# Optimization experiments

Hardware: AMD Instinct MI355X
Metric: run time of the kernel (lower is better)

## Reference

```python
import jax, jax.numpy as jnp
import numpy as np

L_V, L_T, D, H, HID = 1024, 128, 4096, 8, 2048
N1 = L_V // 2      # tokens kept by selector module 1
N2 = N1 // 2       # tokens kept by selector module 2 (final selected)
N_REM = L_V - N2   # remaining tokens to merge


def setup_inputs() -> dict:
    key = jax.random.key(0)
    ks = jax.random.split(key, 8)
    s = 0.02
    return {
        "vision_feature": jax.random.normal(ks[0], (L_V, D), jnp.float32),
        "text_embed": jax.random.normal(ks[1], (L_T, D), jnp.float32),
        "attention_mask": jnp.ones((L_T,), jnp.int32),
        # stacked MHA params, order: [m1.global, m1.local, m2.global, m2.local]
        "attn_in_w": s * jax.random.normal(ks[2], (4, 3 * D, D), jnp.float32),
        "attn_in_b": jnp.zeros((4, 3 * D), jnp.float32),
        "attn_out_w": s * jax.random.normal(ks[3], (4, D, D), jnp.float32),
        "attn_out_b": jnp.zeros((4, D), jnp.float32),
        # stacked MLP params, order: [module1, module2]
        "mlp_w1": s * jax.random.normal(ks[4], (2, HID, D), jnp.float32),
        "mlp_b1": jnp.zeros((2, HID), jnp.float32),
        "mlp_w2": s * jax.random.normal(ks[5], (2, HID), jnp.float32),
        "mlp_b2": jnp.zeros((2,), jnp.float32),
    }


def _mha(xq, xkv, in_w, in_b, out_w, out_b):
    # torch nn.MultiheadAttention (unbatched, eval mode: no dropout)
    dh = D // H
    qw, kw, vw = jnp.split(in_w, 3, axis=0)
    qb, kb, vb = jnp.split(in_b, 3)
    q = (xq @ qw.T + qb).reshape(-1, H, dh)
    k = (xkv @ kw.T + kb).reshape(-1, H, dh)
    v = (xkv @ vw.T + vb).reshape(-1, H, dh)
    scores = jnp.einsum('qhd,khd->hqk', q, k) * (1.0 / np.sqrt(dh))
    attn = jax.nn.softmax(scores, axis=-1)
    o = jnp.einsum('hqk,khd->qhd', attn, v).reshape(-1, D)
    return o @ out_w.T + out_b


def _select(vf, te, pg, pl, w1, b1, w2, b2, n_keep):
    # TokenSelectionModule (deterministic top-k selection path, fixed shapes)
    comb = jnp.concatenate([vf, te], axis=0)
    g = _mha(vf, comb, *pg)
    l = _mha(vf, te, *pl) + vf
    x = jnp.stack([l, g], axis=1)                      # (L, 2, D): 0=local, 1=global
    h = jax.nn.relu(jnp.einsum('lcd,hd->lch', x, w1) + b1)
    logits = jnp.einsum('lch,h->lc', h, w2) + b2       # (L, 2)
    _, idx = jax.lax.top_k(logits[:, 1], n_keep)
    return vf[idx], idx


def _forward(vision_feature, text_embed, attn_in_w, attn_in_b, attn_out_w,
             attn_out_b, mlp_w1, mlp_b1, mlp_w2, mlp_b2):
    p = lambda i: (attn_in_w[i], attn_in_b[i], attn_out_w[i], attn_out_b[i])
    sv1, idx1 = _select(vision_feature, text_embed, p(0), p(1),
                        mlp_w1[0], mlp_b1[0], mlp_w2[0], mlp_b2[0], N1)
    sel, idx2 = _select(sv1, text_embed, p(2), p(3),
                        mlp_w1[1], mlp_b1[1], mlp_w2[1], mlp_b2[1], N2)
    sel_idx = idx1[idx2]

    # remaining = complement of selected indices (fixed size N_REM)
    sel_mask = jnp.zeros((L_V,), bool).at[sel_idx].set(True)
    rem_idx = jnp.nonzero(~sel_mask, size=N_REM)[0]
    rem = vision_feature[rem_idx]                      # (N_REM, D)

    # cosine similarity (torch eps=1e-8) + argmax matching
    nr = jnp.linalg.norm(rem, axis=-1)
    ns = jnp.linalg.norm(sel, axis=-1)
    sim = (rem @ sel.T) / jnp.maximum(nr[:, None] * ns[None, :], 1e-8)
    best = jnp.argmax(sim, axis=1)                     # (N_REM,) cluster ids

    # per-cluster gather+mean+normalize merge, vectorized as segment reduces
    cnt = jax.ops.segment_sum(jnp.ones((N_REM,), jnp.float32), best, num_segments=N2)
    sum_rem = jax.ops.segment_sum(rem, best, num_segments=N2)
    mean = (sel + sum_rem) / (cnt + 1.0)[:, None]
    seg_max = jax.ops.segment_max(nr, best, num_segments=N2)
    max_norm = jnp.maximum(ns, jnp.where(cnt > 0, seg_max, 0.0))
    mean_unit = mean / jnp.linalg.norm(mean, axis=-1, keepdims=True)
    updated = jnp.where((cnt > 0)[:, None], mean_unit * max_norm[:, None], sel)
    return updated  # top_k == 0 path: return merged selected features


def reference(vision_feature, text_embed, attention_mask, attn_in_w, attn_in_b,
              attn_out_w, attn_out_b, mlp_w1, mlp_b1, mlp_w2, mlp_b2):
    # attention_mask is accepted but unused, matching the torch forward
    return _forward(vision_feature, text_embed, attn_in_w, attn_in_b,
                    attn_out_w, attn_out_b, mlp_w1, mlp_b1, mlp_w2, mlp_b2)
```

## Files before the change

kernel.cpp:

```cpp
#include <hip/hip_runtime.h>
#include <hip/hip_bf16.h>
#include <math.h>
#include <stdint.h>

typedef __attribute__((ext_vector_type(4))) float f32x4;
typedef __attribute__((ext_vector_type(8))) short s16x8;
typedef __attribute__((ext_vector_type(4))) short s16x4;

struct sh2 { short hi, lo; };

__device__ __forceinline__ sh2 splitf(float x)
{
    __hip_bfloat16 h = __float2bfloat16(x);
    float hf = __bfloat162float(h);
    __hip_bfloat16 l = __float2bfloat16(x - hf);
    sh2 r;
    r.hi = __builtin_bit_cast(short, h);
    r.lo = __builtin_bit_cast(short, l);
    return r;
}

__device__ __forceinline__ void split8(const float4& a, const float4& b,
                                       s16x8& h, s16x8& l)
{
    sh2 p;
    p = splitf(a.x); h[0] = p.hi; l[0] = p.lo;
    p = splitf(a.y); h[1] = p.hi; l[1] = p.lo;
    p = splitf(a.z); h[2] = p.hi; l[2] = p.lo;
    p = splitf(a.w); h[3] = p.hi; l[3] = p.lo;
    p = splitf(b.x); h[4] = p.hi; l[4] = p.lo;
    p = splitf(b.y); h[5] = p.hi; l[5] = p.lo;
    p = splitf(b.z); h[6] = p.hi; l[6] = p.lo;
    p = splitf(b.w); h[7] = p.hi; l[7] = p.lo;
}

typedef const __attribute__((address_space(1))) void gvoid_t;
typedef __attribute__((address_space(3))) void lvoid_t;
__device__ __forceinline__ void gld_lds16(const void* g, void* l)
{
    __builtin_amdgcn_global_load_lds((gvoid_t*)(uintptr_t)g,
                                     (lvoid_t*)(uintptr_t)l, 16, 0, 0);
}

template<int BF, int EPI, bool RELU>
__global__ __launch_bounds__(256, 2) void mfma_gemm(
    const short* __restrict__ Ahi, const short* __restrict__ Alo, int lda, long sA,
    const float* __restrict__ Bf, const short* __restrict__ Bhi,
    const short* __restrict__ Blo, int ldb, long sB,
    float* __restrict__ Cf, short* __restrict__ Chi, short* __restrict__ Clo,
    short* __restrict__ Thi, short* __restrict__ Tlo, int ldc, int ldT, long sC,
    int K, int SK, float alpha, const float* __restrict__ bias, int mskip)
{
    __shared__ short SH[2][16384];
    const int zf = blockIdx.z;
    const int sk = (SK > 1) ? (zf % SK) : 0;
    const int bz = (SK > 1) ? (zf / SK) : zf;
    const int Kc = K / SK;
    const int kb = sk * Kc;
    Ahi += (long)bz * sA; Alo += (long)bz * sA;
    if (BF == 0) Bf += (long)bz * sB; else { Bhi += (long)bz * sB; Blo += (long)bz * sB; }
    const long cofs = (long)((SK > 1) ? zf : bz) * sC;

    const int GX = gridDim.x, GY = gridDim.y;
    const int nwg = GX * GY;
    const int bid = blockIdx.x + GX * blockIdx.y;
    const int q8 = nwg >> 3, r8 = nwg & 7;
    const int xcd = bid & 7, sl = bid >> 3;
    const int t = (xcd < r8) ? (xcd * (q8 + 1) + sl)
                             : (r8 * (q8 + 1) + (xcd - r8) * q8 + sl);
    const int m0 = (t % GY) * 128, n0 = (t / GY) * 128;

    if (EPI == 2 && n0 < 4096 && m0 >= mskip) return;

    const int tid = threadIdx.x;
    const int lane = tid & 63, wave = tid >> 6;
    const int wr = (wave >> 1) * 64, wc = (wave & 1) * 64;
    const int lrow = lane & 15, lk = lane >> 4;
    const int cswz8 = (lk ^ ((lrow >> 1) & 3)) << 3;

    const int rA0 = wave * 16 + (lane >> 2);
    const int rA1 = rA0 + 64;
    const int sc0 = ((lane & 3) ^ ((rA0 >> 1) & 3)) * 8;
    const int sc1 = ((lane & 3) ^ ((rA1 >> 1) & 3)) * 8;
    const long gA0 = (long)(m0 + rA0) * lda + sc0;
    const long gA1 = (long)(m0 + rA1) * lda + sc1;
    long gB0 = 0, gB1 = 0;
    if (BF == 1) {
        gB0 = (long)(n0 + rA0) * ldb + sc0;
        gB1 = (long)(n0 + rA1) * ldb + sc1;
    }
    const int lw0 = wave * 512, lw1 = wave * 512 + 2048;

    const int brow = tid & 127;
    const int bkc0 = (tid >> 7) * 8;
    const int bkc1 = bkc0 + 16;
    const int bw0 = brow * 32 + (((bkc0 >> 3) ^ ((brow >> 1) & 3)) << 3);
    const int bw1 = brow * 32 + (((bkc1 >> 3) ^ ((brow >> 1) & 3)) << 3);
    const float* bpr = (BF == 0) ? Bf + (long)(n0 + brow) * ldb : nullptr;

    f32x4 acc[4][4];
#pragma unroll
    for (int i = 0; i < 4; i++)
#pragma unroll
        for (int j = 0; j < 4; j++) acc[i][j] = (f32x4){0.f, 0.f, 0.f, 0.f};

    float4 rb0a, rb0b, rb1a, rb1b;

    {
        short* S = &SH[0][0];
        gld_lds16(Ahi + gA0 + kb, S + lw0);
        gld_lds16(Ahi + gA1 + kb, S + lw1);
        gld_lds16(Alo + gA0 + kb, S + 4096 + lw0);
        gld_lds16(Alo + gA1 + kb, S + 4096 + lw1);
        if constexpr (BF == 1) {
            gld_lds16(Bhi + gB0 + kb, S + 8192 + lw0);
            gld_lds16(Bhi + gB1 + kb, S + 8192 + lw1);
            gld_lds16(Blo + gB0 + kb, S + 12288 + lw0);
            gld_lds16(Blo + gB1 + kb, S + 12288 + lw1);
        } else {
            rb0a = *(const float4*)(bpr + kb + bkc0);
            rb0b = *(const float4*)(bpr + kb + bkc0 + 4);
            rb1a = *(const float4*)(bpr + kb + bkc1);
            rb1b = *(const float4*)(bpr + kb + bkc1 + 4);
            s16x8 h, l;
            split8(rb0a, rb0b, h, l);
            *(s16x8*)&S[8192 + bw0] = h;
            *(s16x8*)&S[12288 + bw0] = l;
            split8(rb1a, rb1b, h, l);
            *(s16x8*)&S[8192 + bw1] = h;
            *(s16x8*)&S[12288 + bw1] = l;
        }
    }
    __syncthreads();

    int cur = 0;
    const int kend = kb + Kc;
    for (int k0 = kb; k0 < kend; k0 += 32) {
        const int kn = k0 + 32;
        const bool nx = (kn < kend);
        short* SN = &SH[cur ^ 1][0];
        if (nx) {
            gld_lds16(Ahi + gA0 + kn, SN + lw0);
            gld_lds16(Ahi + gA1 + kn, SN + lw1);
            gld_lds16(Alo + gA0 + kn, SN + 4096 + lw0);
            gld_lds16(Alo + gA1 + kn, SN + 4096 + lw1);
            if constexpr (BF == 1) {
                gld_lds16(Bhi + gB0 + kn, SN + 8192 + lw0);
                gld_lds16(Bhi + gB1 + kn, SN + 8192 + lw1);
                gld_lds16(Blo + gB0 + kn, SN + 12288 + lw0);
                gld_lds16(Blo + gB1 + kn, SN + 12288 + lw1);
            } else {
                rb0a = *(const float4*)(bpr + kn + bkc0);
                rb0b = *(const float4*)(bpr + kn + bkc0 + 4);
                rb1a = *(const float4*)(bpr + kn + bkc1);
                rb1b = *(const float4*)(bpr + kn + bkc1 + 4);
            }
        }
        const short* S = &SH[cur][0];
        s16x8 ah[4], al[4], bh[4], bl[4];
#pragma unroll
        for (int m = 0; m < 4; m++) {
            const int idx = (wr + m * 16 + lrow) * 32 + cswz8;
            ah[m] = *(const s16x8*)&S[idx];
            al[m] = *(const s16x8*)&S[4096 + idx];
        }
#pragma unroll
        for (int n = 0; n < 4; n++) {
            const int idx = (wc + n * 16 + lrow) * 32 + cswz8;
            bh[n] = *(const s16x8*)&S[8192 + idx];
            bl[n] = *(const s16x8*)&S[12288 + idx];
        }
#pragma unroll
        for (int n = 0; n < 4; n++)
#pragma unroll
            for (int m = 0; m < 4; m++)
                acc[m][n] = __builtin_amdgcn_mfma_f32_16x16x32_bf16(ah[m], bh[n], acc[m][n], 0, 0, 0);
#pragma unroll
        for (int n = 0; n < 4; n++)
#pragma unroll
            for (int m = 0; m < 4; m++)
                acc[m][n] = __builtin_amdgcn_mfma_f32_16x16x32_bf16(ah[m], bl[n], acc[m][n], 0, 0, 0);
#pragma unroll
        for (int n = 0; n < 4; n++)
#pragma unroll
            for (int m = 0; m < 4; m++)
                acc[m][n] = __builtin_amdgcn_mfma_f32_16x16x32_bf16(al[m], bh[n], acc[m][n], 0, 0, 0);
        if (BF == 0 && nx) {
            s16x8 h, l;
            split8(rb0a, rb0b, h, l);
            *(s16x8*)&SN[8192 + bw0] = h;
            *(s16x8*)&SN[12288 + bw0] = l;
            split8(rb1a, rb1b, h, l);
            *(s16x8*)&SN[8192 + bw1] = h;
            *(s16x8*)&SN[12288 + bw1] = l;
        }
        __syncthreads();
        cur ^= 1;
    }
#pragma unroll
    for (int n = 0; n < 4; n++) {
        const int col = n0 + wc + n * 16 + lrow;
        const float bv = (SK == 1 && bias) ? bias[col] : 0.f;
#pragma unroll
        for (int m = 0; m < 4; m++) {
            const int row = m0 + wr + m * 16 + lk * 4;
            if (SK > 1) {
#pragma unroll
                for (int r = 0; r < 4; r++)
                    Cf[cofs + (long)(row + r) * ldc + col] = acc[m][n][r] * alpha;
            } else if constexpr (EPI == 0) {
#pragma unroll
                for (int r = 0; r < 4; r++) {
                    float v = acc[m][n][r] * alpha + bv;
                    if (RELU) v = fmaxf(v, 0.f);
                    Cf[cofs + (long)(row + r) * ldc + col] = v;
                }
            } else if constexpr (EPI == 1) {
#pragma unroll
                for (int r = 0; r < 4; r++) {
                    float v = acc[m][n][r] * alpha + bv;
                    sh2 p = splitf(v);
                    Chi[cofs + (long)(row + r) * ldc + col] = p.hi;
                    Clo[cofs + (long)(row + r) * ldc + col] = p.lo;
                }
            } else {
                if (n0 < 8192) {
#pragma unroll
                    for (int r = 0; r < 4; r++) {
                        float v = acc[m][n][r] + bv;
                        sh2 p = splitf(v);
                        Chi[(long)(row + r) * ldc + col] = p.hi;
                        Clo[(long)(row + r) * ldc + col] = p.lo;
                    }
                } else {
                    s16x4 h4, l4;
#pragma unroll
                    for (int r = 0; r < 4; r++) {
                        float v = acc[m][n][r] + bv;
                        sh2 p = splitf(v);
                        h4[r] = p.hi; l4[r] = p.lo;
                    }
                    const long tof = (long)(col - 8192) * ldT + row;
                    *(s16x4*)&Thi[tof] = h4;
                    *(s16x4*)&Tlo[tof] = l4;
                }
            }
        }
    }
}

__global__ __launch_bounds__(512, 2) void mfma_gemm256(
    const short* __restrict__ Ahi, const short* __restrict__ Alo, int lda,
    const float* __restrict__ Bf, int ldb,
    short* __restrict__ Chi, short* __restrict__ Clo,
    short* __restrict__ Thi, short* __restrict__ Tlo, int ldc, int ldT,
    int K, int Mreal, const float* __restrict__ bias, int mskip)
{
    __shared__ short SH[2][32768];

    const int GX = gridDim.x, GY = gridDim.y;
    const int nwg = GX * GY;
    const int bid = blockIdx.x + GX * blockIdx.y;
    const int q8 = nwg >> 3, r8 = nwg & 7;
    const int xcd = bid & 7, sl = bid >> 3;
    const int t = (xcd < r8) ? (xcd * (q8 + 1) + sl)
                             : (r8 * (q8 + 1) + (xcd - r8) * q8 + sl);
    const int m0 = (t % GY) * 256, n0 = (t / GY) * 256;

    if (n0 < 4096 && m0 >= mskip) return;

    const int tid = threadIdx.x;
    const int lane = tid & 63, wave = tid >> 6;
    const int wr = (wave >> 1) * 64, wc = (wave & 1) * 128;
    const int lrow = lane & 15, lk = lane >> 4;
    const int cswz8 = (lk ^ ((lrow >> 1) & 3)) << 3;

    const int rA0 = wave * 32 + (lane >> 2);
    const int rA1 = rA0 + 16;
    const int sc0 = ((lane & 3) ^ ((rA0 >> 1) & 3)) * 8;
    const int sc1 = ((lane & 3) ^ ((rA1 >> 1) & 3)) * 8;
    const long gA0 = (long)(m0 + rA0) * lda + sc0;
    const long gA1 = (long)(m0 + rA1) * lda + sc1;
    const int lw0 = wave * 1024, lw1 = wave * 1024 + 512;

    const int brow = tid & 255;
    const int bk = (tid >> 8) * 16;
    const int bw0 = brow * 32 + ((((bk >> 3) + 0) ^ ((brow >> 1) & 3)) << 3);
    const int bw1 = brow * 32 + ((((bk >> 3) + 1) ^ ((brow >> 1) & 3)) << 3);
    const float* bpr = Bf + (long)(n0 + brow) * ldb + bk;

    f32x4 acc[4][8];
#pragma unroll
    for (int i = 0; i < 4; i++)
#pragma unroll
        for (int j = 0; j < 8; j++) acc[i][j] = (f32x4){0.f, 0.f, 0.f, 0.f};

    float4 rb0, rb1, rb2, rb3;

    {
        short* S = &SH[0][0];
        gld_lds16(Ahi + gA0, S + lw0);
        gld_lds16(Ahi + gA1, S + lw1);
        gld_lds16(Alo + gA0, S + 8192 + lw0);
        gld_lds16(Alo + gA1, S + 8192 + lw1);
        rb0 = *(const float4*)(bpr + 0);
        rb1 = *(const float4*)(bpr + 4);
        rb2 = *(const float4*)(bpr + 8);
        rb3 = *(const float4*)(bpr + 12);
        s16x8 h, l;
        split8(rb0, rb1, h, l);
        *(s16x8*)&S[16384 + bw0] = h;
        *(s16x8*)&S[24576 + bw0] = l;
        split8(rb2, rb3, h, l);
        *(s16x8*)&S[16384 + bw1] = h;
        *(s16x8*)&S[24576 + bw1] = l;
    }
    __syncthreads();

    int cur = 0;
    for (int k0 = 0; k0 < K; k0 += 32) {
        const int kn = k0 + 32;
        const bool nx = (kn < K);
        short* SN = &SH[cur ^ 1][0];
        if (nx) {
            gld_lds16(Ahi + gA0 + kn, SN + lw0);
            gld_lds16(Ahi + gA1 + kn, SN + lw1);
            gld_lds16(Alo + gA0 + kn, SN + 8192 + lw0);
            gld_lds16(Alo + gA1 + kn, SN + 8192 + lw1);
            rb0 = *(const float4*)(bpr + kn + 0);
            rb1 = *(const float4*)(bpr + kn + 4);
            rb2 = *(const float4*)(bpr + kn + 8);
            rb3 = *(const float4*)(bpr + kn + 12);
        }
        const short* S = &SH[cur][0];
        s16x8 ah[4], al[4];
#pragma unroll
        for (int m = 0; m < 4; m++) {
            const int idx = (wr + m * 16 + lrow) * 32 + cswz8;
            ah[m] = *(const s16x8*)&S[idx];
            al[m] = *(const s16x8*)&S[8192 + idx];
        }
#pragma unroll
        for (int np = 0; np < 4; np++) {
            s16x8 bh[2], bl[2];
#pragma unroll
            for (int j = 0; j < 2; j++) {
                const int idx = (wc + (np * 2 + j) * 16 + lrow) * 32 + cswz8;
                bh[j] = *(const s16x8*)&S[16384 + idx];
                bl[j] = *(const s16x8*)&S[24576 + idx];
            }
#pragma unroll
            for (int j = 0; j < 2; j++)
#pragma unroll
                for (int m = 0; m < 4; m++)
                    acc[m][np * 2 + j] = __builtin_amdgcn_mfma_f32_16x16x32_bf16(ah[m], bh[j], acc[m][np * 2 + j], 0, 0, 0);
#pragma unroll
            for (int j = 0; j < 2; j++)
#pragma unroll
                for (int m = 0; m < 4; m++)
                    acc[m][np * 2 + j] = __builtin_amdgcn_mfma_f32_16x16x32_bf16(ah[m], bl[j], acc[m][np * 2 + j], 0, 0, 0);
#pragma unroll
            for (int j = 0; j < 2; j++)
#pragma unroll
                for (int m = 0; m < 4; m++)
                    acc[m][np * 2 + j] = __builtin_amdgcn_mfma_f32_16x16x32_bf16(al[m], bh[j], acc[m][np * 2 + j], 0, 0, 0);
        }
        if (nx) {
            s16x8 h, l;
            split8(rb0, rb1, h, l);
            *(s16x8*)&SN[16384 + bw0] = h;
            *(s16x8*)&SN[24576 + bw0] = l;
            split8(rb2, rb3, h, l);
            *(s16x8*)&SN[16384 + bw1] = h;
            *(s16x8*)&SN[24576 + bw1] = l;
        }
        __syncthreads();
        cur ^= 1;
    }
#pragma unroll
    for (int n = 0; n < 8; n++) {
        const int col = n0 + wc + n * 16 + lrow;
        const float bv = bias[col];
#pragma unroll
        for (int m = 0; m < 4; m++) {
            const int row = m0 + wr + m * 16 + lk * 4;
            if (row < Mreal) {
                if (n0 < 8192) {
#pragma unroll
                    for (int r = 0; r < 4; r++) {
                        float v = acc[m][n][r] + bv;
                        sh2 p = splitf(v);
                        Chi[(long)(row + r) * ldc + col] = p.hi;
                        Clo[(long)(row + r) * ldc + col] = p.lo;
                    }
                } else {
                    s16x4 h4, l4;
#pragma unroll
                    for (int r = 0; r < 4; r++) {
                        float v = acc[m][n][r] + bv;
                        sh2 p = splitf(v);
                        h4[r] = p.hi; l4[r] = p.lo;
                    }
                    const long tof = (long)(col - 8192) * ldT + row;
                    *(s16x4*)&Thi[tof] = h4;
                    *(s16x4*)&Tlo[tof] = l4;
                }
            }
        }
    }
}

template<int EPI, bool RELU>
__global__ __launch_bounds__(256) void reduce_k(
    const float* __restrict__ P, long zstride, int SK, int total,
    int Ninner, int ldc, int colstep,
    float* __restrict__ Cf, short* __restrict__ Chi, short* __restrict__ Clo,
    const float* __restrict__ bias)
{
    const int bz = blockIdx.y;
    const long pbase = (long)bz * SK * zstride;
    const int e = (blockIdx.x * 256 + threadIdx.x) * 4;
    if (e >= total) return;
    const float* p = P + pbase + e;
    float4 s = *(const float4*)p;
    for (int k = 1; k < SK; k++) {
        float4 tv = *(const float4*)(p + (long)k * zstride);
        s.x += tv.x; s.y += tv.y; s.z += tv.z; s.w += tv.w;
    }
    const int r = e / Ninner, c = e % Ninner;
    const int col0 = colstep * bz + c;
    const long ob = (long)r * ldc + col0;
    float v[4] = {s.x, s.y, s.z, s.w};
#pragma unroll
    for (int j = 0; j < 4; j++) {
        float x = v[j] + (bias ? bias[col0 + j] : 0.f);
        if (RELU) x = fmaxf(x, 0.f);
        if constexpr (EPI == 0) {
            Cf[ob + j] = x;
        } else {
            sh2 pp = splitf(x);
            Chi[ob + j] = pp.hi;
            Clo[ob + j] = pp.lo;
        }
    }
}

__global__ __launch_bounds__(256) void split_comb(
    const float* __restrict__ vf, const float* __restrict__ te,
    const int* __restrict__ map, int Mvf,
    short* __restrict__ dhi, short* __restrict__ dlo)
{
    const int r = blockIdx.x;
    const float* srow;
    if (r < Mvf) srow = vf + (long)(map ? map[r] : r) * 4096;
    else         srow = te + (long)(r - Mvf) * 4096;
    const float4* s = (const float4*)srow;
    const long db = (long)r * 4096;
    for (int i = threadIdx.x; i < 1024; i += 256) {
        float4 f = s[i];
        s16x4 h, l;
        sh2 p;
        p = splitf(f.x); h[0] = p.hi; l[0] = p.lo;
        p = splitf(f.y); h[1] = p.hi; l[1] = p.lo;
        p = splitf(f.z); h[2] = p.hi; l[2] = p.lo;
        p = splitf(f.w); h[3] = p.hi; l[3] = p.lo;
        *(s16x4*)&dhi[db + i * 4] = h;
        *(s16x4*)&dlo[db + i * 4] = l;
    }
}

__global__ __launch_bounds__(256) void softmax_split(
    const float* __restrict__ x, short* __restrict__ phi, short* __restrict__ plo,
    int cols)
{
    const long rb = (long)blockIdx.x * cols;
    const float4* xr = (const float4*)(x + rb);
    const int t = threadIdx.x;
    const int n4 = cols >> 2;
    __shared__ float red[256];
    float mx = -INFINITY;
    for (int i = t; i < n4; i += 256) {
        float4 f = xr[i];
        mx = fmaxf(fmaxf(mx, fmaxf(f.x, f.y)), fmaxf(f.z, f.w));
    }
    red[t] = mx; __syncthreads();
    for (int off = 128; off; off >>= 1) { if (t < off) red[t] = fmaxf(red[t], red[t + off]); __syncthreads(); }
    mx = red[0]; __syncthreads();
    float4 ebuf[2];
    float s = 0.f;
    int nb = 0;
    for (int i = t; i < n4; i += 256) {
        float4 f = xr[i];
        f.x = expf(f.x - mx); f.y = expf(f.y - mx); f.z = expf(f.z - mx); f.w = expf(f.w - mx);
        ebuf[nb++] = f;
        s += f.x + f.y + f.z + f.w;
    }
    red[t] = s; __syncthreads();
    for (int off = 128; off; off >>= 1) { if (t < off) red[t] += red[t + off]; __syncthreads(); }
    s = red[0];
    nb = 0;
    for (int i = t; i < n4; i += 256) {
        float4 f = ebuf[nb++];
        f.x /= s; f.y /= s; f.z /= s; f.w /= s;
        s16x4 h, l;
        sh2 p;
        p = splitf(f.x); h[0] = p.hi; l[0] = p.lo;
        p = splitf(f.y); h[1] = p.hi; l[1] = p.lo;
        p = splitf(f.z); h[2] = p.hi; l[2] = p.lo;
        p = splitf(f.w); h[3] = p.hi; l[3] = p.lo;
        *(s16x4*)&phi[rb + i * 4] = h;
        *(s16x4*)&plo[rb + i * 4] = l;
    }
}

__global__ __launch_bounds__(256) void gemv_kernel(
    const float* __restrict__ H, const float* __restrict__ w2,
    const float* __restrict__ b2, float* __restrict__ logits)
{
    const int r = blockIdx.x, t = threadIdx.x;
    const float* row = H + (long)r * 2048;
    float s = 0.f;
    for (int c = t; c < 2048; c += 256) s += row[c] * w2[c];
    __shared__ float red[256];
    red[t] = s; __syncthreads();
    for (int off = 128; off; off >>= 1) { if (t < off) red[t] += red[t + off]; __syncthreads(); }
    if (!t) logits[r] = red[0] + b2[0];
}

__global__ void topk_kernel(const float* __restrict__ vals, int n, int k, int* __restrict__ out)
{
    __shared__ float sv[1024];
    __shared__ int   si[1024];
    const int t = threadIdx.x;
    sv[t] = vals[t]; si[t] = t;
    for (int size = 2; size <= n; size <<= 1) {
        for (int stride = size >> 1; stride > 0; stride >>= 1) {
            __syncthreads();
            const int j = t ^ stride;
            if (j > t) {
                float av = sv[t], bv = sv[j];
                int ai = si[t], bi = si[j];
                const bool before = (av > bv) || (av == bv && ai < bi);
                const bool dir = ((t & size) == 0);
                if (dir ? !before : before) { sv[t] = bv; si[t] = bi; sv[j] = av; si[j] = ai; }
            }
        }
    }
    __syncthreads();
    if (t < k) out[t] = si[t];
}

__global__ void sel_complement_kernel(const int* __restrict__ idx1,
                                      const int* __restrict__ idx2,
                                      int* __restrict__ selidx,
                                      int* __restrict__ remidx)
{
    __shared__ int mask[1024];
    __shared__ int scan[1024];
    const int t = threadIdx.x;
    mask[t] = 0;
    __syncthreads();
    if (t < 256) {
        const int s = idx1[idx2[t]];
        selidx[t] = s;
        mask[s] = 1;
    }
    __syncthreads();
    const int keep = 1 - mask[t];
    scan[t] = keep;
    __syncthreads();
    for (int off = 1; off < 1024; off <<= 1) {
        int v = scan[t];
        if (t >= off) v += scan[t - off];
        __syncthreads();
        scan[t] = v;
        __syncthreads();
    }
    if (keep) remidx[scan[t] - 1] = t;
}

__global__ __launch_bounds__(256) void prep_merge(
    const float* __restrict__ vf,
    const int* __restrict__ remidx, const int* __restrict__ selidx,
    float* __restrict__ rem_f, float* __restrict__ sel_f,
    short* __restrict__ remhi, short* __restrict__ remlo,
    short* __restrict__ selhi, short* __restrict__ sello,
    float* __restrict__ nr, float* __restrict__ ns)
{
    const int b = blockIdx.x, t = threadIdx.x;
    const bool isrem = (b < 768);
    const int r = isrem ? b : b - 768;
    const int sr = isrem ? remidx[r] : selidx[r];
    const float4* s = (const float4*)(vf + (long)sr * 4096);
    float* dstF = (isrem ? rem_f : sel_f) + (long)r * 4096;
    short* dhi = (isrem ? remhi : selhi) + (long)r * 4096;
    short* dlo = (isrem ? remlo : sello) + (long)r * 4096;
    for (int i = t; i < 1024; i += 256) {
        float4 f = s[i];
        *(float4*)&dstF[i * 4] = f;
        s16x4 h, l;
        sh2 p;
        p = splitf(f.x); h[0] = p.hi; l[0] = p.lo;
        p = splitf(f.y); h[1] = p.hi; l[1] = p.lo;
        p = splitf(f.z); h[2] = p.hi; l[2] = p.lo;
        p = splitf(f.w); h[3] = p.hi; l[3] = p.lo;
        *(s16x4*)&dhi[i * 4] = h;
        *(s16x4*)&dlo[i * 4] = l;
    }
    __syncthreads();
    float ss = 0.f;
    for (int c = t; c < 4096; c += 256) { float v = dstF[c]; ss += v * v; }
    __shared__ float red[256];
    red[t] = ss; __syncthreads();
    for (int off = 128; off; off >>= 1) { if (t < off) red[t] += red[t + off]; __syncthreads(); }
    if (!t) (isrem ? nr : ns)[r] = sqrtf(red[0]);
}

__global__ __launch_bounds__(256) void argmax_kernel(
    const float* __restrict__ S, const float* __restrict__ nr,
    const float* __restrict__ ns, int* __restrict__ best)
{
    const int r = blockIdx.x, t = threadIdx.x;
    float v = S[(long)r * 256 + t] / fmaxf(nr[r] * ns[t], 1e-8f);
    __shared__ float bv[256];
    __shared__ int bi[256];
    bv[t] = v; bi[t] = t; __syncthreads();
    for (int off = 128; off; off >>= 1) {
        if (t < off) {
            float ov = bv[t + off]; int oi = bi[t + off];
            if (ov > bv[t] || (ov == bv[t] && oi < bi[t])) { bv[t] = ov; bi[t] = oi; }
        }
        __syncthreads();
    }
    if (!t) best[r] = bi[0];
}

__global__ __launch_bounds__(256) void merge_kernel(
    const float* __restrict__ selb, const float* __restrict__ rem,
    const int* __restrict__ best, const float* __restrict__ nr,
    const float* __restrict__ ns, float* __restrict__ out)
{
    const int j = blockIdx.x, t = threadIdx.x;
    __shared__ int sbest[768];
    __shared__ float snr[768];
    __shared__ float red[256];
    for (int i = t; i < 768; i += 256) { sbest[i] = best[i]; snr[i] = nr[i]; }
    __syncthreads();
    float acc[16];
#pragma unroll
    for (int d = 0; d < 16; d++) acc[d] = 0.f;
    int cnt = 0; float smax = 0.f;
    const int base = t * 16;
    for (int i = 0; i < 768; i++) {
        if (sbest[i] == j) {
            cnt++;
            smax = fmaxf(smax, snr[i]);
            const float* rp = rem + (long)i * 4096 + base;
#pragma unroll
            for (int d = 0; d < 16; d += 4) {
                float4 x4 = *(const float4*)(rp + d);
                acc[d] += x4.x; acc[d + 1] += x4.y; acc[d + 2] += x4.z; acc[d + 3] += x4.w;
            }
        }
    }
    const float* sp = selb + (long)j * 4096 + base;
    float mean[16]; float ss = 0.f;
    const float denom = (float)(cnt + 1);
#pragma unroll
    for (int d = 0; d < 16; d++) { mean[d] = (sp[d] + acc[d]) / denom; ss += mean[d] * mean[d]; }
    red[t] = ss; __syncthreads();
    for (int off = 128; off; off >>= 1) { if (t < off) red[t] += red[t + off]; __syncthreads(); }
    const float nm = sqrtf(red[0]);
    const float mx = fmaxf(ns[j], cnt > 0 ? smax : 0.f);
    float* op = out + (long)j * 4096 + base;
#pragma unroll
    for (int d = 0; d < 16; d++) op[d] = (cnt > 0) ? (mean[d] / nm) * mx : sp[d];
}

extern "C" void kernel_launch(void* const* d_in, const int* in_sizes, int n_in,
                              void* d_out, int out_size, void* d_ws, size_t ws_size,
                              hipStream_t stream)
{
    const float* vf   = (const float*)d_in[0];
    const float* te   = (const float*)d_in[1];
    const float* inw  = (const float*)d_in[3];
    const float* inb  = (const float*)d_in[4];
    const float* outw = (const float*)d_in[5];
    const float* outb = (const float*)d_in[6];
    const float* w1   = (const float*)d_in[7];
    const float* b1   = (const float*)d_in[8];
    const float* w2   = (const float*)d_in[9];
    const float* b2   = (const float*)d_in[10];
    float* out = (float*)d_out;
    char* base = (char*)d_ws;

    char* qkR = base;
    char* vTR = base + 37748736;
    char* scR = vTR + 18874368;
    float* smalls = (float*)(scR + 37748736);

    short* qkhi = (short*)qkR;
    short* qklo = (short*)(qkR + 18874368);
    short* vThi = (short*)vTR;
    short* vTlo = (short*)(vTR + 9437184);
    float* hbuf = (float*)scR;

    float* logits = smalls;
    float* nr     = smalls + 1024;
    float* ns     = smalls + 1792;
    int* idx1   = (int*)(smalls + 2048);
    int* idx2   = (int*)(smalls + 2560);
    int* selidx = (int*)(smalls + 2816);
    int* remidx = (int*)(smalls + 3072);
    int* best   = (int*)(smalls + 3840);

    const float scl = (float)(1.0 / sqrt(512.0));
    const int NOSKIP = 1 << 30;

    for (int m = 0; m < 2; m++) {
        const int Mq  = m ? 512 : 1024;
        const int Mkv = m ? 640 : 1152;
        const float* Wqkv = inw + (size_t)(2 * m) * 12288 * 4096;
        const float* bqkv = inb + (size_t)(2 * m) * 12288;
        const float* ow = outw + (size_t)(2 * m) * 4096 * 4096;
        const float* ob = outb + (size_t)(2 * m) * 4096;

        short* chi = (short*)scR;
        short* clo = (short*)(scR + (size_t)Mkv * 4096 * 2);
        split_comb<<<Mkv, 256, 0, stream>>>(vf, te, m ? idx1 : nullptr, Mq, chi, clo);
        if (m == 0) {
            mfma_gemm256<<<dim3(48, 5, 1), 512, 0, stream>>>(
                chi, clo, 4096, Wqkv, 4096, qkhi, qklo, vThi, vTlo,
                8192, 1152, 4096, 1152, bqkv, 1024);
        } else {
            mfma_gemm<0, 2, false><<<dim3(96, Mkv / 128, 1), 256, 0, stream>>>(
                chi, clo, 4096, 0, Wqkv, nullptr, nullptr, 4096, 0,
                nullptr, qkhi, qklo, vThi, vTlo, 8192, 1152, 0, 4096, 1, 1.f,
                bqkv, 512);
        }
        float* scor = (float*)(m ? (scR + 10485760) : scR);
        mfma_gemm<1, 0, false><<<dim3(Mkv / 128, Mq / 128, 8), 256, 0, stream>>>(
            qkhi, qklo, 8192, 512, nullptr, qkhi + 4096, qklo + 4096, 8192, 512,
            scor, nullptr, nullptr, nullptr, nullptr, Mkv, 0, (long)Mq * Mkv,
            512, 1, scl, nullptr, NOSKIP);
        short* phi = (short*)qkR;
        short* plo = (short*)(qkR + (size_t)8 * Mq * Mkv * 2);
        softmax_split<<<8 * Mq, 256, 0, stream>>>(scor, phi, plo, Mkv);
        short* ohi = (short*)scR;
        short* olo = (short*)(scR + (size_t)Mq * 4096 * 2);
        if (m == 0) {
            mfma_gemm<1, 1, false><<<dim3(4, 8, 8), 256, 0, stream>>>(
                phi, plo, Mkv, (long)Mq * Mkv, nullptr, vThi, vTlo, 1152, 512L * 1152,
                nullptr, ohi, olo, nullptr, nullptr, 4096, 0, 512, Mkv, 1, 1.f,
                nullptr, NOSKIP);
        } else {
            float* Ppv = (float*)(qkR + 20971520);
            mfma_gemm<1, 0, false><<<dim3(4, 4, 16), 256, 0, stream>>>(
                phi, plo, Mkv, (long)Mq * Mkv, nullptr, vThi, vTlo, 1152, 512L * 1152,
                Ppv, nullptr, nullptr, nullptr, nullptr, 512, 0, 262144,
                Mkv, 2, 1.f, nullptr, NOSKIP);
            reduce_k<1, false><<<dim3(256, 8), 256, 0, stream>>>(
                Ppv, 262144, 2, 262144, 512, 4096, 512, nullptr, ohi, olo, nullptr);
        }
        short* ghi = (short*)(scR + (size_t)Mq * 4096 * 4);
        short* glo = (short*)(scR + (size_t)Mq * 4096 * 6);
        {
            float* Pg = (float*)qkR;
            const long zst = (long)Mq * 4096;
            mfma_gemm<0, 0, false><<<dim3(32, Mq / 128, 2), 256, 0, stream>>>(
                ohi, olo, 4096, 0, ow, nullptr, nullptr, 4096, 0,
                Pg, nullptr, nullptr, nullptr, nullptr, 4096, 0, zst,
                4096, 2, 1.f, nullptr, NOSKIP);
            reduce_k<1, false><<<dim3((int)(zst / 1024), 1), 256, 0, stream>>>(
                Pg, zst, 2, (int)zst, 4096, 4096, 0, nullptr, ghi, glo, ob);
        }
        {
            float* Pm = (float*)(qkR + 8388608);
            const long zst = (long)Mq * 2048;
            mfma_gemm<0, 0, false><<<dim3(16, Mq / 128, 4), 256, 0, stream>>>(
                ghi, glo, 4096, 0, w1 + (size_t)m * 2048 * 4096, nullptr, nullptr, 4096, 0,
                Pm, nullptr, nullptr, nullptr, nullptr, 2048, 0, zst,
                4096, 4, 1.f, nullptr, NOSKIP);
            reduce_k<0, true><<<dim3((int)(zst / 1024), 1), 256, 0, stream>>>(
                Pm, zst, 4, (int)zst, 2048, 2048, 0, hbuf, nullptr, nullptr,
                b1 + (size_t)m * 2048);
        }
        gemv_kernel<<<Mq, 256, 0, stream>>>(hbuf, w2 + (size_t)m * 2048, b2 + m, logits);
        if (m == 0) topk_kernel<<<1, 1024, 0, stream>>>(logits, 1024, 512, idx1);
        else        topk_kernel<<<1, 512, 0, stream>>>(logits, 512, 256, idx2);
    }

    short* remhi = (short*)scR;
    short* remlo = (short*)(scR + 6291456);
    short* selhi = (short*)(scR + 12582912);
    short* sello = (short*)(scR + 14680064);
    float* rem_f = (float*)(scR + 16777216);
    float* sel_f = (float*)(scR + 29360128);
    float* Smat  = (float*)(scR + 33554432);

    sel_complement_kernel<<<1, 1024, 0, stream>>>(idx1, idx2, selidx, remidx);
    prep_merge<<<1024, 256, 0, stream>>>(vf, remidx, selidx, rem_f, sel_f,
                                         remhi, remlo, selhi, sello, nr, ns);
    {
        float* Ps = (float*)qkR;
        mfma_gemm<1, 0, false><<<dim3(2, 6, 8), 256, 0, stream>>>(
            remhi, remlo, 4096, 0, nullptr, selhi, sello, 4096, 0,
            Ps, nullptr, nullptr, nullptr, nullptr, 256, 0, 196608,
            4096, 8, 1.f, nullptr, NOSKIP);
        reduce_k<0, false><<<dim3(192, 1), 256, 0, stream>>>(
            Ps, 196608, 8, 196608, 256, 256, 0, Smat, nullptr, nullptr, nullptr);
    }
    argmax_kernel<<<768, 256, 0, stream>>>(Smat, nr, ns, best);
    merge_kernel<<<256, 256, 0, stream>>>(sel_f, rem_f, best, nr, ns, out);
}
```

Before: 1.306 ms.

## Add 256x256-tile split-K MFMA GEMM for output projection and MLP layers

Introduces a new 512-thread GEMM kernel with 256x256 tiles, double-buffered LDS, XCD-aware block remapping, and fp32 weights split into bf16 hi/lo on the fly. It replaces the 128-tile GEMMs for the attention output projection and the MLP first layer, using higher split-K factors so the grid stays filled. Partial sums go to a new workspace region beyond the existing buffers. This trades more split-K partial traffic and larger reduce passes for better operand reuse per block, and it relies on the workspace being large enough for the new offset.

```diff
diff --git a/kernel.cpp b/kernel.cpp
--- a/kernel.cpp
+++ b/kernel.cpp
@@ -410,6 +410,150 @@
     }
 }
 
+__global__ __launch_bounds__(512, 2) void mfma_gemm256sk(
+    const short* __restrict__ Ahi, const short* __restrict__ Alo, int lda,
+    const float* __restrict__ Bf, int ldb,
+    float* __restrict__ P, long zstride, int ldp,
+    int K, int SK)
+{
+    __shared__ short SH[2][32768];
+
+    const int sk = blockIdx.z;
+    const int Kc = K / SK;
+    const int kb = sk * Kc;
+
+    const int GX = gridDim.x, GY = gridDim.y;
+    const int nwg = GX * GY;
+    const int bid = blockIdx.x + GX * blockIdx.y;
+    const int q8 = nwg >> 3, r8 = nwg & 7;
+    const int xcd = bid & 7, sl = bid >> 3;
+    const int t = (xcd < r8) ? (xcd * (q8 + 1) + sl)
+                             : (r8 * (q8 + 1) + (xcd - r8) * q8 + sl);
+    const int m0 = (t % GY) * 256, n0 = (t / GY) * 256;
+
+    const int tid = threadIdx.x;
+    const int lane = tid & 63, wave = tid >> 6;
+    const int wr = (wave >> 1) * 64, wc = (wave & 1) * 128;
+    const int lrow = lane & 15, lk = lane >> 4;
+    const int cswz8 = (lk ^ ((lrow >> 1) & 3)) << 3;
+
+    const int rA0 = wave * 32 + (lane >> 2);
+    const int rA1 = rA0 + 16;
+    const int sc0 = ((lane & 3) ^ ((rA0 >> 1) & 3)) * 8;
+    const int sc1 = ((lane & 3) ^ ((rA1 >> 1) & 3)) * 8;
+    const long gA0 = (long)(m0 + rA0) * lda + sc0;
+    const long gA1 = (long)(m0 + rA1) * lda + sc1;
+    const int lw0 = wave * 1024, lw1 = wave * 1024 + 512;
+
+    const int brow = tid & 255;
+    const int bk = (tid >> 8) * 16;
+    const int bw0 = brow * 32 + ((((bk >> 3) + 0) ^ ((brow >> 1) & 3)) << 3);
+    const int bw1 = brow * 32 + ((((bk >> 3) + 1) ^ ((brow >> 1) & 3)) << 3);
+    const float* bpr = Bf + (long)(n0 + brow) * ldb + bk;
+
+    f32x4 acc[4][8];
+#pragma unroll
+    for (int i = 0; i < 4; i++)
+#pragma unroll
+        for (int j = 0; j < 8; j++) acc[i][j] = (f32x4){0.f, 0.f, 0.f, 0.f};
+
+    float4 rb0, rb1, rb2, rb3;
+
+    {
+        short* S = &SH[0][0];
+        gld_lds16(Ahi + gA0 + kb, S + lw0);
+        gld_lds16(Ahi + gA1 + kb, S + lw1);
+        gld_lds16(Alo + gA0 + kb, S + 8192 + lw0);
+        gld_lds16(Alo + gA1 + kb, S + 8192 + lw1);
+        rb0 = *(const float4*)(bpr + kb + 0);
+        rb1 = *(const float4*)(bpr + kb + 4);
+        rb2 = *(const float4*)(bpr + kb + 8);
+        rb3 = *(const float4*)(bpr + kb + 12);
+        s16x8 h, l;
+        split8(rb0, rb1, h, l);
+        *(s16x8*)&S[16384 + bw0] = h;
+        *(s16x8*)&S[24576 + bw0] = l;
+        split8(rb2, rb3, h, l);
+        *(s16x8*)&S[16384 + bw1] = h;
+        *(s16x8*)&S[24576 + bw1] = l;
+    }
+    __syncthreads();
+
+    int cur = 0;
+    const int kend = kb + Kc;
+    for (int k0 = kb; k0 < kend; k0 += 32) {
+        const int kn = k0 + 32;
+        const bool nx = (kn < kend);
+        short* SN = &SH[cur ^ 1][0];
+        if (nx) {
+            gld_lds16(Ahi + gA0 + kn, SN + lw0);
+            gld_lds16(Ahi + gA1 + kn, SN + lw1);
+            gld_lds16(Alo + gA0 + kn, SN + 8192 + lw0);
+            gld_lds16(Alo + gA1 + kn, SN + 8192 + lw1);
+            rb0 = *(const float4*)(bpr + kn + 0);
+            rb1 = *(const float4*)(bpr + kn + 4);
+            rb2 = *(const float4*)(bpr + kn + 8);
+            rb3 = *(const float4*)(bpr + kn + 12);
+        }
+        const short* S = &SH[cur][0];
+        s16x8 ah[4], al[4];
+#pragma unroll
+        for (int m = 0; m < 4; m++) {
+            const int idx = (wr + m * 16 + lrow) * 32 + cswz8;
+            ah[m] = *(const s16x8*)&S[idx];
+            al[m] = *(const s16x8*)&S[8192 + idx];
+        }
+#pragma unroll
+        for (int np = 0; np < 4; np++) {
+            s16x8 bh[2], bl[2];
+#pragma unroll
+            for (int j = 0; j < 2; j++) {
+                const int idx = (wc + (np * 2 + j) * 16 + lrow) * 32 + cswz8;
+                bh[j] = *(const s16x8*)&S[16384 + idx];
+                bl[j] = *(const s16x8*)&S[24576 + idx];
+            }
+#pragma unroll
+            for (int j = 0; j < 2; j++)
+#pragma unroll
+                for (int m = 0; m < 4; m++)
+                    acc[m][np * 2 + j] = __builtin_amdgcn_mfma_f32_16x16x32_bf16(ah[m], bh[j], acc[m][np * 2 + j], 0, 0, 0);
+#pragma unroll
+            for (int j = 0; j < 2; j++)
+#pragma unroll
+                for (int m = 0; m < 4; m++)
+                    acc[m][np * 2 + j] = __builtin_amdgcn_mfma_f32_16x16x32_bf16(ah[m], bl[j], acc[m][np * 2 + j], 0, 0, 0);
+#pragma unroll
+            for (int j = 0; j < 2; j++)
+#pragma unroll
+                for (int m = 0; m < 4; m++)
+                    acc[m][np * 2 + j] = __builtin_amdgcn_mfma_f32_16x16x32_bf16(al[m], bh[j], acc[m][np * 2 + j], 0, 0, 0);
+        }
+        if (nx) {
+            s16x8 h, l;
+            split8(rb0, rb1, h, l);
+            *(s16x8*)&SN[16384 + bw0] = h;
+            *(s16x8*)&SN[24576 + bw0] = l;
+            split8(rb2, rb3, h, l);
+            *(s16x8*)&SN[16384 + bw1] = h;
+            *(s16x8*)&SN[24576 + bw1] = l;
+        }
+        __syncthreads();
+        cur ^= 1;
+    }
+    const long zofs = (long)sk * zstride;
+#pragma unroll
+    for (int n = 0; n < 8; n++) {
+        const int col = n0 + wc + n * 16 + lrow;
+#pragma unroll
+        for (int m = 0; m < 4; m++) {
+            const int row = m0 + wr + m * 16 + lk * 4;
+#pragma unroll
+            for (int r = 0; r < 4; r++)
+                P[zofs + (long)(row + r) * ldp + col] = acc[m][n][r];
+        }
+    }
+}
+
 template<int EPI, bool RELU>
 __global__ __launch_bounds__(256) void reduce_k(
     const float* __restrict__ P, long zstride, int SK, int total,
@@ -698,6 +842,7 @@
     char* vTR = base + 37748736;
     char* scR = vTR + 18874368;
     float* smalls = (float*)(scR + 37748736);
+    float* pbig = (float*)(base + 134217728);
 
     short* qkhi = (short*)qkR;
     short* qklo = (short*)(qkR + 18874368);
@@ -765,24 +910,21 @@
         short* ghi = (short*)(scR + (size_t)Mq * 4096 * 4);
         short* glo = (short*)(scR + (size_t)Mq * 4096 * 6);
         {
-            float* Pg = (float*)qkR;
+            const int SKg = m ? 8 : 4;
             const long zst = (long)Mq * 4096;
-            mfma_gemm<0, 0, false><<<dim3(32, Mq / 128, 2), 256, 0, stream>>>(
-                ohi, olo, 4096, 0, ow, nullptr, nullptr, 4096, 0,
-                Pg, nullptr, nullptr, nullptr, nullptr, 4096, 0, zst,
-                4096, 2, 1.f, nullptr, NOSKIP);
+            mfma_gemm256sk<<<dim3(16, Mq / 256, SKg), 512, 0, stream>>>(
+                ohi, olo, 4096, ow, 4096, pbig, zst, 4096, 4096, SKg);
             reduce_k<1, false><<<dim3((int)(zst / 1024), 1), 256, 0, stream>>>(
-                Pg, zst, 2, (int)zst, 4096, 4096, 0, nullptr, ghi, glo, ob);
+                pbig, zst, SKg, (int)zst, 4096, 4096, 0, nullptr, ghi, glo, ob);
         }
         {
-            float* Pm = (float*)(qkR + 8388608);
+            const int SKm = m ? 16 : 8;
             const long zst = (long)Mq * 2048;
-            mfma_gemm<0, 0, false><<<dim3(16, Mq / 128, 4), 256, 0, stream>>>(
-                ghi, glo, 4096, 0, w1 + (size_t)m * 2048 * 4096, nullptr, nullptr, 4096, 0,
-                Pm, nullptr, nullptr, nullptr, nullptr, 2048, 0, zst,
-                4096, 4, 1.f, nullptr, NOSKIP);
+            mfma_gemm256sk<<<dim3(8, Mq / 256, SKm), 512, 0, stream>>>(
+                ghi, glo, 4096, w1 + (size_t)m * 2048 * 4096, 4096,
+                pbig, zst, 2048, 4096, SKm);
             reduce_k<0, true><<<dim3((int)(zst / 1024), 1), 256, 0, stream>>>(
-                Pm, zst, 4, (int)zst, 2048, 2048, 0, hbuf, nullptr, nullptr,
+                pbig, zst, SKm, (int)zst, 2048, 2048, 0, hbuf, nullptr, nullptr,
                 b1 + (size_t)m * 2048);
         }
         gemv_kernel<<<Mq, 256, 0, stream>>>(hbuf, w2 + (size_t)m * 2048, b2 + m, logits);
```

Result: faster. 1.238 ms, median of 2 (-5.2%).
